# Performance work log

Measured on AMD Instinct MI355X. Metric: run time of the kernel, lower is better.

The kernel has to match this reference:

```python
import jax, jax.numpy as jnp
import numpy as np

NUM_EXPERTS = 4096
NUM_KEYS = 64  # floor(sqrt(num_experts))
TOP_K = 16
NORM_TOPK = False
BN_EPS = 1e-5


def setup_inputs() -> dict:
    key = jax.random.key(0)
    ks = jax.random.split(key, 7)
    B, S, H, I = 2, 2048, 2048, 8192
    s = 0.02
    return {
        "hidden_states": jax.random.normal(ks[0], (B, S, H), jnp.float32),
        "router_gate_w": jax.random.normal(ks[1], (2 * NUM_KEYS, H), jnp.float32) * s,
        "down_embed": jax.random.normal(ks[2], (NUM_EXPERTS, H), jnp.float32) * s,
        "up_embed": jax.random.normal(ks[3], (NUM_EXPERTS, H), jnp.float32) * s,
        "gate_w": jax.random.normal(ks[4], (I, H), jnp.float32) * s,
        "up_w": jax.random.normal(ks[5], (I, H), jnp.float32) * s,
        "down_w": jax.random.normal(ks[6], (H, I), jnp.float32) * s,
    }


def reference(hidden_states, router_gate_w, down_embed, up_embed, gate_w, up_w, down_w):
    B, S, H = hidden_states.shape
    x = hidden_states.reshape(-1, H)  # [N, H]

    # BatchNorm1d(affine=False), training-mode batch statistics (biased var)
    mu = jnp.mean(x, axis=0, keepdims=True)
    var = jnp.mean(jnp.square(x - mu), axis=0, keepdims=True)
    xn = (x - mu) * jax.lax.rsqrt(var + BN_EPS)

    # product-key router: logits [2, N, num_keys]
    rlog = (xn @ router_gate_w.T).reshape(-1, 2, NUM_KEYS).transpose(1, 0, 2)
    logp = jax.nn.log_softmax(rlog, axis=-1)

    # full product scores [N, nk, nk]; top-k over nk*nk candidates
    full = logp[0][:, :, None] + logp[1][:, None, :]
    scores, indices = jax.lax.top_k(full.reshape(-1, NUM_KEYS * NUM_KEYS), TOP_K)
    routing_weights = jnp.exp(scores)  # [N, k]
    if NORM_TOPK:
        routing_weights = routing_weights / jnp.sum(routing_weights, axis=-1, keepdims=True)

    # PEER-style expert: scalar key match then weighted up-embedding sum
    d = down_embed[indices]  # [N, k, H]
    u = up_embed[indices]    # [N, k, H]
    h = jnp.einsum('nh,nkh->nk', x, d)
    experts_states = jnp.einsum('nk,nk,nkh->nh', routing_weights, h, u)

    # dense gated MLP (silu)
    mlp = (jax.nn.silu(x @ gate_w.T) * (x @ up_w.T)) @ down_w.T

    out = (mlp + experts_states).reshape(B, S, H)
    return out, rlog
```

## Files before the change

### kernel.cpp

```cpp
#include <hip/hip_runtime.h>
#include <stdint.h>

#define H_DIM 2048
#define N_TOK 4096
#define I_DIM 8192

typedef __attribute__((ext_vector_type(8))) short short8;
typedef __attribute__((ext_vector_type(4))) float f32x4;

typedef const __attribute__((address_space(1))) unsigned int* gp_t;
typedef __attribute__((address_space(3))) unsigned int* lp_t;

__device__ __forceinline__ void gload16(const unsigned short* g, short* l) {
    __builtin_amdgcn_global_load_lds((gp_t)g, (lp_t)l, 16, 0, 0);
}

__device__ __forceinline__ unsigned short f2bf(float f) {
    union { float f; unsigned int u; } c; c.f = f;
    unsigned int u = c.u;
    return (unsigned short)((u + 0x7FFFu + ((u >> 16) & 1u)) >> 16);
}
__device__ __forceinline__ float bf2f(unsigned short u) {
    union { unsigned int i; float f; } c; c.i = ((unsigned int)u) << 16;
    return c.f;
}

__device__ __forceinline__ float wmax64(float v) {
#pragma unroll
    for (int o = 32; o > 0; o >>= 1) v = fmaxf(v, __shfl_xor(v, o));
    return v;
}
__device__ __forceinline__ float wsum64(float v) {
#pragma unroll
    for (int o = 32; o > 0; o >>= 1) v += __shfl_xor(v, o);
    return v;
}

template<int K, int RSTEP, int LSTEP>
__device__ __forceinline__ void stage4(const unsigned short* src, short* dst) {
#pragma unroll
    for (int j = 0; j < 4; ++j)
        gload16(src + (size_t)j * RSTEP * K, dst + j * LSTEP);
}

__global__ __launch_bounds__(256) void bn_stats(const float* __restrict__ x,
                                                float* __restrict__ ps, float* __restrict__ pq) {
    int col = blockIdx.x * 256 + threadIdx.x;
    int r0  = blockIdx.y * 128;
    float s = 0.f, q = 0.f;
    for (int r = 0; r < 128; ++r) {
        float v = x[(size_t)(r0 + r) * H_DIM + col];
        s += v; q += v * v;
    }
    ps[blockIdx.y * H_DIM + col] = s;
    pq[blockIdx.y * H_DIM + col] = q;
}

__global__ __launch_bounds__(256) void bn_finalize(const float* __restrict__ ps, const float* __restrict__ pq,
                                                   float* __restrict__ mu, float* __restrict__ rsig) {
    int c = blockIdx.x * 256 + threadIdx.x;
    float s = 0.f, q = 0.f;
    for (int i = 0; i < 32; ++i) { s += ps[i * H_DIM + c]; q += pq[i * H_DIM + c]; }
    float m = s * (1.f / N_TOK);
    float v = q * (1.f / N_TOK) - m * m;
    mu[c] = m;
    rsig[c] = rsqrtf(v + 1e-5f);
}

__global__ __launch_bounds__(256) void cvt_x(const float* __restrict__ x, unsigned short* __restrict__ xb) {
    size_t i = ((size_t)blockIdx.x * 256 + threadIdx.x) * 4;
    float4 v = *(const float4*)(x + i);
    uint2 o;
    o.x = (unsigned)f2bf(v.x) | ((unsigned)f2bf(v.y) << 16);
    o.y = (unsigned)f2bf(v.z) | ((unsigned)f2bf(v.w) << 16);
    *(uint2*)(xb + i) = o;
}

__global__ __launch_bounds__(256) void cvt_w(const float* __restrict__ src, unsigned short* __restrict__ dst) {
    size_t off = ((size_t)blockIdx.x * 256 + threadIdx.x) * 8;
    float4 a = *(const float4*)(src + off);
    float4 b = *(const float4*)(src + off + 4);
    short8 s;
    s[0]=(short)f2bf(a.x); s[1]=(short)f2bf(a.y); s[2]=(short)f2bf(a.z); s[3]=(short)f2bf(a.w);
    s[4]=(short)f2bf(b.x); s[5]=(short)f2bf(b.y); s[6]=(short)f2bf(b.z); s[7]=(short)f2bf(b.w);
    *(short8*)(dst + off) = s;
}

__global__ __launch_bounds__(256) void router_kernel(const float* __restrict__ x, const float* __restrict__ rgw,
                                                     const float* __restrict__ mu, const float* __restrict__ rsig,
                                                     float* __restrict__ rlog) {
    __shared__ float xs[16][65];
    __shared__ float rs[128][65];
    const int t = threadIdx.x;
    const int n0 = blockIdx.x * 16;
    const int tk = t >> 5;
    const int jj = t & 31;
    float acc[2][4] = {{0.f,0.f,0.f,0.f},{0.f,0.f,0.f,0.f}};

    for (int kc = 0; kc < H_DIM; kc += 64) {
        {
            int row = t >> 4, c4 = (t & 15) * 4;
            float4 v = *(const float4*)(x + (size_t)(n0 + row) * H_DIM + kc + c4);
            float4 m = *(const float4*)(mu + kc + c4);
            float4 r = *(const float4*)(rsig + kc + c4);
            xs[row][c4 + 0] = (v.x - m.x) * r.x;
            xs[row][c4 + 1] = (v.y - m.y) * r.y;
            xs[row][c4 + 2] = (v.z - m.z) * r.z;
            xs[row][c4 + 3] = (v.w - m.w) * r.w;
        }
        {
            int row = t >> 1, base = (t & 1) * 32;
            const float* src = rgw + (size_t)row * H_DIM + kc + base;
#pragma unroll
            for (int i = 0; i < 8; ++i) {
                float4 v = *(const float4*)(src + i * 4);
                rs[row][base + i*4 + 0] = v.x;
                rs[row][base + i*4 + 1] = v.y;
                rs[row][base + i*4 + 2] = v.z;
                rs[row][base + i*4 + 3] = v.w;
            }
        }
        __syncthreads();
#pragma unroll 4
        for (int k = 0; k < 64; ++k) {
            float x0 = xs[tk][k], x1 = xs[tk + 8][k];
            float r0 = rs[jj][k], r1 = rs[jj + 32][k], r2 = rs[jj + 64][k], r3 = rs[jj + 96][k];
            acc[0][0] += x0 * r0; acc[0][1] += x0 * r1; acc[0][2] += x0 * r2; acc[0][3] += x0 * r3;
            acc[1][0] += x1 * r0; acc[1][1] += x1 * r1; acc[1][2] += x1 * r2; acc[1][3] += x1 * r3;
        }
        __syncthreads();
    }
#pragma unroll
    for (int a = 0; a < 2; ++a)
#pragma unroll
        for (int b = 0; b < 4; ++b) {
            int n = n0 + tk + 8 * a;
            int j = jj + 32 * b;
            rlog[(size_t)(j >> 6) * (N_TOK * 64) + (size_t)n * 64 + (j & 63)] = acc[a][b];
        }
}

__global__ __launch_bounds__(256) void topk_kernel(const float* __restrict__ rlog,
                                                   float* __restrict__ topw, int* __restrict__ topi) {
    const int lane = threadIdx.x & 63;
    const int n = blockIdx.x * 4 + (threadIdx.x >> 6);

    float a = rlog[(size_t)n * 64 + lane];
    float b = rlog[(size_t)(N_TOK * 64) + (size_t)n * 64 + lane];
    float ma = wmax64(a);
    float lpa = a - ma - logf(wsum64(expf(a - ma)));
    float mb = wmax64(b);
    float lpb = b - mb - logf(wsum64(expf(b - mb)));

    float va = lpa, vb = lpb;
    float tva = -1e30f, tvb = -1e30f; int tia = 0, tib = 0;
    for (int it = 0; it < 16; ++it) {
        float mx = wmax64(va);
        int w = __ffsll(__ballot(va == mx)) - 1;
        if (lane == it) { tva = mx; tia = w; }
        if (lane == w) va = -1e30f;
        mx = wmax64(vb);
        w = __ffsll(__ballot(vb == mx)) - 1;
        if (lane == it) { tvb = mx; tib = w; }
        if (lane == w) vb = -1e30f;
    }
    float av = __shfl(tva, lane >> 2);
    int   ai = __shfl(tia, lane >> 2);
    int   q0 = (lane & 3) * 4;
    float c0 = av + __shfl(tvb, q0 + 0); int b0 = __shfl(tib, q0 + 0);
    float c1 = av + __shfl(tvb, q0 + 1); int b1 = __shfl(tib, q0 + 1);
    float c2 = av + __shfl(tvb, q0 + 2); int b2 = __shfl(tib, q0 + 2);
    float c3 = av + __shfl(tvb, q0 + 3); int b3 = __shfl(tib, q0 + 3);

    for (int it = 0; it < 16; ++it) {
        float lv = c0; int lq = 0;
        if (c1 > lv) { lv = c1; lq = 1; }
        if (c2 > lv) { lv = c2; lq = 2; }
        if (c3 > lv) { lv = c3; lq = 3; }
        float mx = wmax64(lv);
        int w = __ffsll(__ballot(lv == mx)) - 1;
        if (lane == w) {
            int bj;
            switch (lq) {
                case 0:  bj = b0; c0 = -1e30f; break;
                case 1:  bj = b1; c1 = -1e30f; break;
                case 2:  bj = b2; c2 = -1e30f; break;
                default: bj = b3; c3 = -1e30f; break;
            }
            topw[n * 16 + it] = expf(mx);
            topi[n * 16 + it] = ai * 64 + bj;
        }
    }
}

__global__ __launch_bounds__(256) void experts_kernel(const float* __restrict__ x, const float* __restrict__ de,
                                                      const float* __restrict__ ue, const float* __restrict__ topw,
                                                      const int* __restrict__ topi, float* __restrict__ out) {
    __shared__ float psum[16][4];
    const int n = blockIdx.x;
    const int t = threadIdx.x, lane = t & 63, wid = t >> 6;

    float xr[8];
    {
        float4 v0 = *(const float4*)(x + (size_t)n * H_DIM + t * 8);
        float4 v1 = *(const float4*)(x + (size_t)n * H_DIM + t * 8 + 4);
        xr[0]=v0.x; xr[1]=v0.y; xr[2]=v0.z; xr[3]=v0.w;
        xr[4]=v1.x; xr[5]=v1.y; xr[6]=v1.z; xr[7]=v1.w;
    }
    int   eidx[16];
    float ew[16];
#pragma unroll
    for (int k = 0; k < 16; ++k) { eidx[k] = topi[n * 16 + k]; ew[k] = topw[n * 16 + k]; }

#pragma unroll
    for (int k = 0; k < 16; ++k) {
        const float* dr = de + (size_t)eidx[k] * H_DIM + t * 8;
        float4 v0 = *(const float4*)dr;
        float4 v1 = *(const float4*)(dr + 4);
        float p = v0.x*xr[0] + v0.y*xr[1] + v0.z*xr[2] + v0.w*xr[3]
                + v1.x*xr[4] + v1.y*xr[5] + v1.z*xr[6] + v1.w*xr[7];
        p = wsum64(p);
        if (lane == 0) psum[k][wid] = p;
    }
    __syncthreads();

    float acc[8] = {0,0,0,0,0,0,0,0};
#pragma unroll
    for (int k = 0; k < 16; ++k) {
        float h = psum[k][0] + psum[k][1] + psum[k][2] + psum[k][3];
        float coef = ew[k] * h;
        const float* ur = ue + (size_t)eidx[k] * H_DIM + t * 8;
        float4 v0 = *(const float4*)ur;
        float4 v1 = *(const float4*)(ur + 4);
        acc[0] += coef * v0.x; acc[1] += coef * v0.y; acc[2] += coef * v0.z; acc[3] += coef * v0.w;
        acc[4] += coef * v1.x; acc[5] += coef * v1.y; acc[6] += coef * v1.z; acc[7] += coef * v1.w;
    }
    float4 o0 = {acc[0], acc[1], acc[2], acc[3]};
    float4 o1 = {acc[4], acc[5], acc[6], acc[7]};
    *(float4*)(out + (size_t)n * H_DIM + t * 8)     = o0;
    *(float4*)(out + (size_t)n * H_DIM + t * 8 + 4) = o1;
}

#define SWZB(row, byteoff) ((byteoff) ^ (((row) & 7) << 4))

#define NT256 (H_DIM / 64)

__global__ __launch_bounds__(512, 2) void gemm256(const unsigned short* __restrict__ Amat,
                                                  const unsigned short* __restrict__ Bmat,
                                                  unsigned short* __restrict__ act, int mode) {
    __shared__ __attribute__((aligned(16))) short sA[2][16384];
    __shared__ __attribute__((aligned(16))) short sB[2][16384];
    const int t = threadIdx.x;
    const int lane = t & 63, wid = t >> 6;
    const int wm = wid >> 2, wn = wid & 3;
    const int l15 = lane & 15, l4 = lane >> 4;
    const int bid = blockIdx.x;
    const int sw = (bid & 7) * 64 + (bid >> 3);
    const int bx = sw & 31, by = sw >> 5;
    const int row0 = by * 256, col0 = bx * 256;

    const int rseg = lane >> 3;
    const int chunk = (lane & 7) ^ rseg;
    const unsigned short* aSrc = Amat + (size_t)(row0 + wid * 8 + rseg) * H_DIM + chunk * 8;
    const unsigned short* bSrc = Bmat + (size_t)(col0 + wid * 8 + rseg) * H_DIM + chunk * 8;

    const int swzb = (l15 & 7) << 4;
    const int kx0 = (l4 * 16) ^ swzb;
    const int kx1 = (64 + l4 * 16) ^ swzb;
    const int arow = (wm * 128 + l15) * 64;
    const int brow = (wn * 64 + l15) * 64;

    f32x4 zero = {0.f, 0.f, 0.f, 0.f};
    f32x4 acc[8][4];
#pragma unroll
    for (int m = 0; m < 8; ++m)
#pragma unroll
        for (int n = 0; n < 4; ++n) acc[m][n] = zero;

    stage4<H_DIM, 64, 4096>(aSrc,      &sA[0][wid * 512]);
    stage4<H_DIM, 64, 4096>(bSrc,      &sB[0][wid * 512]);
    stage4<H_DIM, 64, 4096>(aSrc + 64, &sA[1][wid * 512]);
    stage4<H_DIM, 64, 4096>(bSrc + 64, &sB[1][wid * 512]);
    asm volatile("s_waitcnt vmcnt(8)" ::: "memory");
    __builtin_amdgcn_s_barrier();
    asm volatile("" ::: "memory");

    for (int g = 0; g < NT256; ++g) {
        const int c = g & 1;
        const short* Ac = &sA[c][0];
        const short* Bc = &sB[c][0];
        short8 a0[4], a0h[4], a1[4], a1h[4], b0[4], b1[4];
#pragma unroll
        for (int m = 0; m < 4; ++m) a0[m]  = *(const short8*)(Ac + arow + m * 1024 + (kx0 >> 1));
#pragma unroll
        for (int m = 0; m < 4; ++m) a0h[m] = *(const short8*)(Ac + arow + (m + 4) * 1024 + (kx0 >> 1));
#pragma unroll
        for (int n = 0; n < 4; ++n) b0[n]  = *(const short8*)(Bc + brow + n * 1024 + (kx0 >> 1));
        __builtin_amdgcn_s_setprio(1);
#pragma unroll
        for (int m = 0; m < 4; ++m)
#pragma unroll
            for (int n = 0; n < 4; ++n)
                acc[m][n] = __builtin_amdgcn_mfma_f32_16x16x32_bf16(a0[m], b0[n], acc[m][n], 0, 0, 0);
        __builtin_amdgcn_s_setprio(0);
        asm volatile("" ::: "memory");
        __builtin_amdgcn_s_barrier();
        asm volatile("" ::: "memory");
#pragma unroll
        for (int m = 0; m < 4; ++m) a1[m]  = *(const short8*)(Ac + arow + m * 1024 + (kx1 >> 1));
#pragma unroll
        for (int m = 0; m < 4; ++m) a1h[m] = *(const short8*)(Ac + arow + (m + 4) * 1024 + (kx1 >> 1));
#pragma unroll
        for (int n = 0; n < 4; ++n) b1[n]  = *(const short8*)(Bc + brow + n * 1024 + (kx1 >> 1));
        __builtin_amdgcn_s_setprio(1);
#pragma unroll
        for (int m = 0; m < 4; ++m)
#pragma unroll
            for (int n = 0; n < 4; ++n)
                acc[m + 4][n] = __builtin_amdgcn_mfma_f32_16x16x32_bf16(a0h[m], b0[n], acc[m + 4][n], 0, 0, 0);
        __builtin_amdgcn_s_setprio(0);
        asm volatile("s_waitcnt lgkmcnt(0)" ::: "memory");
        __builtin_amdgcn_s_barrier();
        asm volatile("" ::: "memory");
        if (g + 2 < NT256) stage4<H_DIM, 64, 4096>(aSrc + (size_t)(g + 2) * 64, &sA[c][wid * 512]);
        __builtin_amdgcn_s_setprio(1);
#pragma unroll
        for (int m = 0; m < 4; ++m)
#pragma unroll
            for (int n = 0; n < 4; ++n)
                acc[m][n] = __builtin_amdgcn_mfma_f32_16x16x32_bf16(a1[m], b1[n], acc[m][n], 0, 0, 0);
        __builtin_amdgcn_s_setprio(0);
        asm volatile("" ::: "memory");
        __builtin_amdgcn_s_barrier();
        asm volatile("" ::: "memory");
        if (g + 2 < NT256) stage4<H_DIM, 64, 4096>(bSrc + (size_t)(g + 2) * 64, &sB[c][wid * 512]);
        __builtin_amdgcn_s_setprio(1);
#pragma unroll
        for (int m = 0; m < 4; ++m)
#pragma unroll
            for (int n = 0; n < 4; ++n)
                acc[m + 4][n] = __builtin_amdgcn_mfma_f32_16x16x32_bf16(a1h[m], b1[n], acc[m + 4][n], 0, 0, 0);
        __builtin_amdgcn_s_setprio(0);
        if (g + 2 < NT256) { asm volatile("s_waitcnt vmcnt(8)" ::: "memory"); }
        else               { asm volatile("s_waitcnt vmcnt(0)" ::: "memory"); }
        __builtin_amdgcn_s_barrier();
        asm volatile("" ::: "memory");
    }

    const int rbase = row0 + wm * 128, cbase = col0 + wn * 64;
    if (mode == 0) {
#pragma unroll
        for (int m = 0; m < 8; ++m)
#pragma unroll
            for (int n = 0; n < 4; ++n)
#pragma unroll
                for (int j = 0; j < 4; ++j) {
                    int r = rbase + m * 16 + l4 * 4 + j;
                    int c2 = cbase + n * 16 + l15;
                    act[(size_t)r * I_DIM + c2] = f2bf(acc[m][n][j]);
                }
    } else {
#pragma unroll
        for (int m = 0; m < 8; ++m)
#pragma unroll
            for (int n = 0; n < 4; ++n)
#pragma unroll
                for (int j = 0; j < 4; ++j) {
                    int r = rbase + m * 16 + l4 * 4 + j;
                    int c2 = cbase + n * 16 + l15;
                    size_t idx = (size_t)r * I_DIM + c2;
                    float gv = bf2f(act[idx]);
                    float uv = acc[m][n][j];
                    float sv = gv / (1.f + expf(-gv));
                    act[idx] = f2bf(sv * uv);
                }
    }
}

#define NTD (I_DIM / 64)

__global__ __launch_bounds__(256, 2) void gemm_down128(const unsigned short* __restrict__ act,
                                                       const unsigned short* __restrict__ dwb,
                                                       float* __restrict__ out) {
    __shared__ __attribute__((aligned(16))) short sA[2][8192];
    __shared__ __attribute__((aligned(16))) short sB[2][8192];
    const int t = threadIdx.x;
    const int lane = t & 63, wid = t >> 6;
    const int wm = wid >> 1, wn = wid & 1;
    const int l15 = lane & 15, l4 = lane >> 4;
    const int bid = blockIdx.x;
    const int sw = (bid & 7) * 64 + (bid >> 3);
    const int bx = sw & 15, by = sw >> 4;
    const int row0 = by * 128, col0 = bx * 128;

    const int rseg = lane >> 3;
    const int chunk = (lane & 7) ^ rseg;
    const unsigned short* aSrc = act + (size_t)(row0 + wid * 8 + rseg) * I_DIM + chunk * 8;
    const unsigned short* bSrc = dwb + (size_t)(col0 + wid * 8 + rseg) * I_DIM + chunk * 8;

    const int swzb = (l15 & 7) << 4;
    const int kx0 = (l4 * 16) ^ swzb;
    const int kx1 = (64 + l4 * 16) ^ swzb;
    const int arow = (wm * 64 + l15) * 64;
    const int brow = (wn * 64 + l15) * 64;

    f32x4 zero = {0.f, 0.f, 0.f, 0.f};
    f32x4 acc[4][4];
#pragma unroll
    for (int m = 0; m < 4; ++m)
#pragma unroll
        for (int n = 0; n < 4; ++n) acc[m][n] = zero;

    stage4<I_DIM, 32, 2048>(aSrc,      &sA[0][wid * 512]);
    stage4<I_DIM, 32, 2048>(bSrc,      &sB[0][wid * 512]);
    stage4<I_DIM, 32, 2048>(aSrc + 64, &sA[1][wid * 512]);
    stage4<I_DIM, 32, 2048>(bSrc + 64, &sB[1][wid * 512]);
    asm volatile("s_waitcnt vmcnt(8)" ::: "memory");
    __builtin_amdgcn_s_barrier();
    asm volatile("" ::: "memory");

    for (int g = 0; g < NTD; ++g) {
        const int c = g & 1;
        const short* Ac = &sA[c][0];
        const short* Bc = &sB[c][0];
        short8 a0[4], a1[4], b0[4], b1[4];
#pragma unroll
        for (int m = 0; m < 4; ++m) a0[m] = *(const short8*)(Ac + arow + m * 1024 + (kx0 >> 1));
#pragma unroll
        for (int n = 0; n < 4; ++n) b0[n] = *(const short8*)(Bc + brow + n * 1024 + (kx0 >> 1));
#pragma unroll
        for (int m = 0; m < 4; ++m) a1[m] = *(const short8*)(Ac + arow + m * 1024 + (kx1 >> 1));
#pragma unroll
        for (int n = 0; n < 4; ++n) b1[n] = *(const short8*)(Bc + brow + n * 1024 + (kx1 >> 1));
        __builtin_amdgcn_s_setprio(1);
#pragma unroll
        for (int m = 0; m < 4; ++m)
#pragma unroll
            for (int n = 0; n < 4; ++n)
                acc[m][n] = __builtin_amdgcn_mfma_f32_16x16x32_bf16(a0[m], b0[n], acc[m][n], 0, 0, 0);
        __builtin_amdgcn_s_setprio(0);
        asm volatile("s_waitcnt lgkmcnt(0)" ::: "memory");
        __builtin_amdgcn_s_barrier();
        asm volatile("" ::: "memory");
        if (g + 2 < NTD) {
            stage4<I_DIM, 32, 2048>(aSrc + (size_t)(g + 2) * 64, &sA[c][wid * 512]);
            stage4<I_DIM, 32, 2048>(bSrc + (size_t)(g + 2) * 64, &sB[c][wid * 512]);
        }
        __builtin_amdgcn_s_setprio(1);
#pragma unroll
        for (int m = 0; m < 4; ++m)
#pragma unroll
            for (int n = 0; n < 4; ++n)
                acc[m][n] = __builtin_amdgcn_mfma_f32_16x16x32_bf16(a1[m], b1[n], acc[m][n], 0, 0, 0);
        __builtin_amdgcn_s_setprio(0);
        if (g + 2 < NTD) { asm volatile("s_waitcnt vmcnt(8)" ::: "memory"); }
        else             { asm volatile("s_waitcnt vmcnt(0)" ::: "memory"); }
        __builtin_amdgcn_s_barrier();
        asm volatile("" ::: "memory");
    }

    const int rbase = row0 + wm * 64, cbase = col0 + wn * 64;
#pragma unroll
    for (int m = 0; m < 4; ++m)
#pragma unroll
        for (int n = 0; n < 4; ++n)
#pragma unroll
            for (int j = 0; j < 4; ++j) {
                int r = rbase + m * 16 + l4 * 4 + j;
                int c2 = cbase + n * 16 + l15;
                out[(size_t)r * H_DIM + c2] += acc[m][n][j];
            }
}

__global__ __launch_bounds__(256) void gemm_gu(const unsigned short* __restrict__ xb,
                                               const float* __restrict__ gw, const float* __restrict__ uw,
                                               unsigned short* __restrict__ act) {
    __shared__ __attribute__((aligned(16))) short As[128 * 64];
    __shared__ __attribute__((aligned(16))) short Bg[128 * 64];
    __shared__ __attribute__((aligned(16))) short Bu[128 * 64];
    const int t = threadIdx.x;
    const int lane = t & 63, wid = t >> 6;
    const int wr = wid >> 1, wc = wid & 1;
    const int l15 = lane & 15, l4 = lane >> 4;
    const int row0 = blockIdx.y * 128;
    const int col0 = blockIdx.x * 128;
    const int srow = t >> 1, shalf = (t & 1) * 32;

    f32x4 zero = {0.f, 0.f, 0.f, 0.f};
    f32x4 accg[4][4], accu[4][4];
#pragma unroll
    for (int m = 0; m < 4; ++m)
#pragma unroll
        for (int n = 0; n < 4; ++n) { accg[m][n] = zero; accu[m][n] = zero; }

    for (int kt = 0; kt < H_DIM; kt += 64) {
        {
            const unsigned short* src = xb + (size_t)(row0 + srow) * H_DIM + kt + shalf;
#pragma unroll
            for (int i = 0; i < 4; ++i) {
                int boff = SWZB(srow, (shalf + i * 8) * 2);
                *(short8*)(As + srow * 64 + (boff >> 1)) = *(const short8*)(src + i * 8);
            }
        }
        {
            const float* g = gw + (size_t)(col0 + srow) * H_DIM + kt + shalf;
            const float* u = uw + (size_t)(col0 + srow) * H_DIM + kt + shalf;
#pragma unroll
            for (int i = 0; i < 4; ++i) {
                int boff = SWZB(srow, (shalf + i * 8) * 2);
                float4 a0 = *(const float4*)(g + i * 8);
                float4 a1 = *(const float4*)(g + i * 8 + 4);
                short8 s;
                s[0]=(short)f2bf(a0.x); s[1]=(short)f2bf(a0.y); s[2]=(short)f2bf(a0.z); s[3]=(short)f2bf(a0.w);
                s[4]=(short)f2bf(a1.x); s[5]=(short)f2bf(a1.y); s[6]=(short)f2bf(a1.z); s[7]=(short)f2bf(a1.w);
                *(short8*)(Bg + srow * 64 + (boff >> 1)) = s;
                float4 b0 = *(const float4*)(u + i * 8);
                float4 b1 = *(const float4*)(u + i * 8 + 4);
                short8 r;
                r[0]=(short)f2bf(b0.x); r[1]=(short)f2bf(b0.y); r[2]=(short)f2bf(b0.z); r[3]=(short)f2bf(b0.w);
                r[4]=(short)f2bf(b1.x); r[5]=(short)f2bf(b1.y); r[6]=(short)f2bf(b1.z); r[7]=(short)f2bf(b1.w);
                *(short8*)(Bu + srow * 64 + (boff >> 1)) = r;
            }
        }
        __syncthreads();
#pragma unroll
        for (int kk = 0; kk < 64; kk += 32) {
            short8 af[4], bgf[4], buf_[4];
#pragma unroll
            for (int m = 0; m < 4; ++m) {
                int row = wr * 64 + m * 16 + l15;
                af[m] = *(const short8*)(As + row * 64 + (SWZB(row, (kk + l4 * 8) * 2) >> 1));
            }
#pragma unroll
            for (int n = 0; n < 4; ++n) {
                int row = wc * 64 + n * 16 + l15;
                int off = row * 64 + (SWZB(row, (kk + l4 * 8) * 2) >> 1);
                bgf[n]  = *(const short8*)(Bg + off);
                buf_[n] = *(const short8*)(Bu + off);
            }
#pragma unroll
            for (int m = 0; m < 4; ++m)
#pragma unroll
                for (int n = 0; n < 4; ++n) {
                    accg[m][n] = __builtin_amdgcn_mfma_f32_16x16x32_bf16(af[m], bgf[n],  accg[m][n], 0, 0, 0);
                    accu[m][n] = __builtin_amdgcn_mfma_f32_16x16x32_bf16(af[m], buf_[n], accu[m][n], 0, 0, 0);
                }
        }
        __syncthreads();
    }
    const int rbase = row0 + wr * 64, cbase = col0 + wc * 64;
#pragma unroll
    for (int m = 0; m < 4; ++m)
#pragma unroll
        for (int n = 0; n < 4; ++n)
#pragma unroll
            for (int j = 0; j < 4; ++j) {
                int r = rbase + m * 16 + l4 * 4 + j;
                int c = cbase + n * 16 + l15;
                float gv = accg[m][n][j];
                float uv = accu[m][n][j];
                float sv = gv / (1.f + expf(-gv));
                act[(size_t)r * I_DIM + c] = f2bf(sv * uv);
            }
}

__global__ __launch_bounds__(256) void gemm_down(const unsigned short* __restrict__ act,
                                                 const float* __restrict__ dw, float* __restrict__ out) {
    __shared__ __attribute__((aligned(16))) short As[128 * 64];
    __shared__ __attribute__((aligned(16))) short Bs[128 * 64];
    const int t = threadIdx.x;
    const int lane = t & 63, wid = t >> 6;
    const int wr = wid >> 1, wc = wid & 1;
    const int l15 = lane & 15, l4 = lane >> 4;
    const int row0 = blockIdx.y * 128;
    const int col0 = blockIdx.x * 128;
    const int srow = t >> 1, shalf = (t & 1) * 32;

    f32x4 zero = {0.f, 0.f, 0.f, 0.f};
    f32x4 acc[4][4];
#pragma unroll
    for (int m = 0; m < 4; ++m)
#pragma unroll
        for (int n = 0; n < 4; ++n) acc[m][n] = zero;

    for (int kt = 0; kt < I_DIM; kt += 64) {
        {
            const unsigned short* src = act + (size_t)(row0 + srow) * I_DIM + kt + shalf;
#pragma unroll
            for (int i = 0; i < 4; ++i) {
                int boff = SWZB(srow, (shalf + i * 8) * 2);
                *(short8*)(As + srow * 64 + (boff >> 1)) = *(const short8*)(src + i * 8);
            }
        }
        {
            const float* g = dw + (size_t)(col0 + srow) * I_DIM + kt + shalf;
#pragma unroll
            for (int i = 0; i < 4; ++i) {
                int boff = SWZB(srow, (shalf + i * 8) * 2);
                float4 a0 = *(const float4*)(g + i * 8);
                float4 a1 = *(const float4*)(g + i * 8 + 4);
                short8 s;
                s[0]=(short)f2bf(a0.x); s[1]=(short)f2bf(a0.y); s[2]=(short)f2bf(a0.z); s[3]=(short)f2bf(a0.w);
                s[4]=(short)f2bf(a1.x); s[5]=(short)f2bf(a1.y); s[6]=(short)f2bf(a1.z); s[7]=(short)f2bf(a1.w);
                *(short8*)(Bs + srow * 64 + (boff >> 1)) = s;
            }
        }
        __syncthreads();
#pragma unroll
        for (int kk = 0; kk < 64; kk += 32) {
            short8 af[4], bf[4];
#pragma unroll
            for (int m = 0; m < 4; ++m) {
                int row = wr * 64 + m * 16 + l15;
                af[m] = *(const short8*)(As + row * 64 + (SWZB(row, (kk + l4 * 8) * 2) >> 1));
            }
#pragma unroll
            for (int n = 0; n < 4; ++n) {
                int row = wc * 64 + n * 16 + l15;
                bf[n] = *(const short8*)(Bs + row * 64 + (SWZB(row, (kk + l4 * 8) * 2) >> 1));
            }
#pragma unroll
            for (int m = 0; m < 4; ++m)
#pragma unroll
                for (int n = 0; n < 4; ++n)
                    acc[m][n] = __builtin_amdgcn_mfma_f32_16x16x32_bf16(af[m], bf[n], acc[m][n], 0, 0, 0);
        }
        __syncthreads();
    }
    const int rbase = row0 + wr * 64, cbase = col0 + wc * 64;
#pragma unroll
    for (int m = 0; m < 4; ++m)
#pragma unroll
        for (int n = 0; n < 4; ++n)
#pragma unroll
            for (int j = 0; j < 4; ++j) {
                int r = rbase + m * 16 + l4 * 4 + j;
                int c = cbase + n * 16 + l15;
                out[(size_t)r * H_DIM + c] += acc[m][n][j];
            }
}

extern "C" void kernel_launch(void* const* d_in, const int* in_sizes, int n_in,
                              void* d_out, int out_size, void* d_ws, size_t ws_size,
                              hipStream_t stream) {
    const float* x   = (const float*)d_in[0];
    const float* rgw = (const float*)d_in[1];
    const float* de  = (const float*)d_in[2];
    const float* ue  = (const float*)d_in[3];
    const float* gw  = (const float*)d_in[4];
    const float* uw  = (const float*)d_in[5];
    const float* dw  = (const float*)d_in[6];
    float* out = (float*)d_out;
    char* ws = (char*)d_ws;

    float* ps   = (float*)(ws + 0);
    float* pq   = (float*)(ws + 262144);
    float* mu   = (float*)(ws + 524288);
    float* rsig = (float*)(ws + 532480);
    float* topw = (float*)(ws + 540672);
    int*   topi = (int*)  (ws + 802816);
    unsigned short* xb  = (unsigned short*)(ws + 1179648);
    unsigned short* act = (unsigned short*)(ws + 17956864);
    unsigned short* gwb = (unsigned short*)(ws + 85065728);
    unsigned short* uwb = (unsigned short*)(ws + 118620160);
    unsigned short* dwb = (unsigned short*)(ws + 152174592);
    float* rlog = out + 8388608;
    const bool fast = ws_size >= 185729024ULL;

    bn_stats   <<<dim3(8, 32), 256, 0, stream>>>(x, ps, pq);
    bn_finalize<<<8, 256, 0, stream>>>(ps, pq, mu, rsig);
    cvt_x      <<<8192, 256, 0, stream>>>(x, xb);
    router_kernel<<<256, 256, 0, stream>>>(x, rgw, mu, rsig, rlog);
    topk_kernel<<<1024, 256, 0, stream>>>(rlog, topw, topi);
    experts_kernel<<<4096, 256, 0, stream>>>(x, de, ue, topw, topi, out);

    if (fast) {
        cvt_w<<<8192, 256, 0, stream>>>(gw, gwb);
        cvt_w<<<8192, 256, 0, stream>>>(uw, uwb);
        cvt_w<<<8192, 256, 0, stream>>>(dw, dwb);
        gemm256<<<512, 512, 0, stream>>>(xb, gwb, act, 0);
        gemm256<<<512, 512, 0, stream>>>(xb, uwb, act, 1);
        gemm_down128<<<512, 256, 0, stream>>>(act, dwb, out);
    } else {
        gemm_gu    <<<dim3(64, 32), 256, 0, stream>>>(xb, gw, uw, act);
        gemm_down  <<<dim3(16, 32), 256, 0, stream>>>(act, dw, out);
    }
}
```

Measured before the change: 846.1 us.

## Fuse bf16 conversions, use bf16 expert embeddings, simplify GEMM double buffering

Merges all fp32-to-bf16 conversions (weights, expert embeddings, x) into one launch. Adds a bf16 variant of the experts kernel that gathers down/up embeddings at half the bytes. Replaces the hand-scheduled two-stage-ahead prefetch with split barriers in the gate/up and down GEMMs with a simpler one-ahead double buffer and __syncthreads. The simpler pipeline may hide less load latency, and the extra embedding conversion adds traffic and lowers expert precision.

```diff
diff --git a/kernel.cpp b/kernel.cpp
--- a/kernel.cpp
+++ b/kernel.cpp
@@ -65,6 +65,29 @@
     float v = q * (1.f / N_TOK) - m * m;
     mu[c] = m;
     rsig[c] = rsqrtf(v + 1e-5f);
+}
+
+__global__ __launch_bounds__(256) void cvt_all(const float* __restrict__ gw, const float* __restrict__ uw,
+                                               const float* __restrict__ dw, const float* __restrict__ de,
+                                               const float* __restrict__ ue, const float* __restrict__ x,
+                                               unsigned short* __restrict__ gwb, unsigned short* __restrict__ uwb,
+                                               unsigned short* __restrict__ dwb, unsigned short* __restrict__ deb,
+                                               unsigned short* __restrict__ ueb, unsigned short* __restrict__ xb) {
+    int b = blockIdx.x;
+    const float* src; unsigned short* dst; size_t base;
+    if      (b < 8192)  { src = gw; dst = gwb; base = (size_t)b; }
+    else if (b < 16384) { src = uw; dst = uwb; base = (size_t)(b - 8192); }
+    else if (b < 24576) { src = dw; dst = dwb; base = (size_t)(b - 16384); }
+    else if (b < 28672) { src = de; dst = deb; base = (size_t)(b - 24576); }
+    else if (b < 32768) { src = ue; dst = ueb; base = (size_t)(b - 28672); }
+    else                { src = x;  dst = xb;  base = (size_t)(b - 32768); }
+    size_t off = (base * 256 + threadIdx.x) * 8;
+    float4 a = *(const float4*)(src + off);
+    float4 c = *(const float4*)(src + off + 4);
+    short8 s;
+    s[0]=(short)f2bf(a.x); s[1]=(short)f2bf(a.y); s[2]=(short)f2bf(a.z); s[3]=(short)f2bf(a.w);
+    s[4]=(short)f2bf(c.x); s[5]=(short)f2bf(c.y); s[6]=(short)f2bf(c.z); s[7]=(short)f2bf(c.w);
+    *(short8*)(dst + off) = s;
 }
 
 __global__ __launch_bounds__(256) void cvt_x(const float* __restrict__ x, unsigned short* __restrict__ xb) {
@@ -193,6 +216,51 @@
     }
 }
 
+__global__ __launch_bounds__(256) void experts_kernel_b(const float* __restrict__ x, const unsigned short* __restrict__ de,
+                                                        const unsigned short* __restrict__ ue, const float* __restrict__ topw,
+                                                        const int* __restrict__ topi, float* __restrict__ out) {
+    __shared__ float psum[16][4];
+    const int n = blockIdx.x;
+    const int t = threadIdx.x, lane = t & 63, wid = t >> 6;
+
+    float xr[8];
+    {
+        float4 v0 = *(const float4*)(x + (size_t)n * H_DIM + t * 8);
+        float4 v1 = *(const float4*)(x + (size_t)n * H_DIM + t * 8 + 4);
+        xr[0]=v0.x; xr[1]=v0.y; xr[2]=v0.z; xr[3]=v0.w;
+        xr[4]=v1.x; xr[5]=v1.y; xr[6]=v1.z; xr[7]=v1.w;
+    }
+    int   eidx[16];
+    float ew[16];
+#pragma unroll
+    for (int k = 0; k < 16; ++k) { eidx[k] = topi[n * 16 + k]; ew[k] = topw[n * 16 + k]; }
+
+#pragma unroll
+    for (int k = 0; k < 16; ++k) {
+        short8 d = *(const short8*)(de + (size_t)eidx[k] * H_DIM + t * 8);
+        float p = 0.f;
+#pragma unroll
+        for (int j = 0; j < 8; ++j) p += bf2f((unsigned short)d[j]) * xr[j];
+        p = wsum64(p);
+        if (lane == 0) psum[k][wid] = p;
+    }
+    __syncthreads();
+
+    float acc[8] = {0,0,0,0,0,0,0,0};
+#pragma unroll
+    for (int k = 0; k < 16; ++k) {
+        float h = psum[k][0] + psum[k][1] + psum[k][2] + psum[k][3];
+        float coef = ew[k] * h;
+        short8 u = *(const short8*)(ue + (size_t)eidx[k] * H_DIM + t * 8);
+#pragma unroll
+        for (int j = 0; j < 8; ++j) acc[j] += coef * bf2f((unsigned short)u[j]);
+    }
+    float4 o0 = {acc[0], acc[1], acc[2], acc[3]};
+    float4 o1 = {acc[4], acc[5], acc[6], acc[7]};
+    *(float4*)(out + (size_t)n * H_DIM + t * 8)     = o0;
+    *(float4*)(out + (size_t)n * H_DIM + t * 8 + 4) = o1;
+}
+
 __global__ __launch_bounds__(256) void experts_kernel(const float* __restrict__ x, const float* __restrict__ de,
                                                       const float* __restrict__ ue, const float* __restrict__ topw,
                                                       const int* __restrict__ topi, float* __restrict__ out) {
@@ -277,74 +345,62 @@
 #pragma unroll
         for (int n = 0; n < 4; ++n) acc[m][n] = zero;
 
-    stage4<H_DIM, 64, 4096>(aSrc,      &sA[0][wid * 512]);
-    stage4<H_DIM, 64, 4096>(bSrc,      &sB[0][wid * 512]);
-    stage4<H_DIM, 64, 4096>(aSrc + 64, &sA[1][wid * 512]);
-    stage4<H_DIM, 64, 4096>(bSrc + 64, &sB[1][wid * 512]);
-    asm volatile("s_waitcnt vmcnt(8)" ::: "memory");
-    __builtin_amdgcn_s_barrier();
-    asm volatile("" ::: "memory");
-
+    stage4<H_DIM, 64, 4096>(aSrc, &sA[0][wid * 512]);
+    stage4<H_DIM, 64, 4096>(bSrc, &sB[0][wid * 512]);
+    __syncthreads();
+
+    int cur = 0;
     for (int g = 0; g < NT256; ++g) {
-        const int c = g & 1;
-        const short* Ac = &sA[c][0];
-        const short* Bc = &sB[c][0];
-        short8 a0[4], a0h[4], a1[4], a1h[4], b0[4], b1[4];
-#pragma unroll
-        for (int m = 0; m < 4; ++m) a0[m]  = *(const short8*)(Ac + arow + m * 1024 + (kx0 >> 1));
-#pragma unroll
-        for (int m = 0; m < 4; ++m) a0h[m] = *(const short8*)(Ac + arow + (m + 4) * 1024 + (kx0 >> 1));
-#pragma unroll
-        for (int n = 0; n < 4; ++n) b0[n]  = *(const short8*)(Bc + brow + n * 1024 + (kx0 >> 1));
-        __builtin_amdgcn_s_setprio(1);
-#pragma unroll
-        for (int m = 0; m < 4; ++m)
-#pragma unroll
-            for (int n = 0; n < 4; ++n)
-                acc[m][n] = __builtin_amdgcn_mfma_f32_16x16x32_bf16(a0[m], b0[n], acc[m][n], 0, 0, 0);
-        __builtin_amdgcn_s_setprio(0);
-        asm volatile("" ::: "memory");
-        __builtin_amdgcn_s_barrier();
-        asm volatile("" ::: "memory");
-#pragma unroll
-        for (int m = 0; m < 4; ++m) a1[m]  = *(const short8*)(Ac + arow + m * 1024 + (kx1 >> 1));
-#pragma unroll
-        for (int m = 0; m < 4; ++m) a1h[m] = *(const short8*)(Ac + arow + (m + 4) * 1024 + (kx1 >> 1));
-#pragma unroll
-        for (int n = 0; n < 4; ++n) b1[n]  = *(const short8*)(Bc + brow + n * 1024 + (kx1 >> 1));
-        __builtin_amdgcn_s_setprio(1);
-#pragma unroll
-        for (int m = 0; m < 4; ++m)
-#pragma unroll
-            for (int n = 0; n < 4; ++n)
-                acc[m + 4][n] = __builtin_amdgcn_mfma_f32_16x16x32_bf16(a0h[m], b0[n], acc[m + 4][n], 0, 0, 0);
-        __builtin_amdgcn_s_setprio(0);
-        asm volatile("s_waitcnt lgkmcnt(0)" ::: "memory");
-        __builtin_amdgcn_s_barrier();
-        asm volatile("" ::: "memory");
-        if (g + 2 < NT256) stage4<H_DIM, 64, 4096>(aSrc + (size_t)(g + 2) * 64, &sA[c][wid * 512]);
-        __builtin_amdgcn_s_setprio(1);
-#pragma unroll
-        for (int m = 0; m < 4; ++m)
-#pragma unroll
-            for (int n = 0; n < 4; ++n)
-                acc[m][n] = __builtin_amdgcn_mfma_f32_16x16x32_bf16(a1[m], b1[n], acc[m][n], 0, 0, 0);
-        __builtin_amdgcn_s_setprio(0);
-        asm volatile("" ::: "memory");
-        __builtin_amdgcn_s_barrier();
-        asm volatile("" ::: "memory");
-        if (g + 2 < NT256) stage4<H_DIM, 64, 4096>(bSrc + (size_t)(g + 2) * 64, &sB[c][wid * 512]);
-        __builtin_amdgcn_s_setprio(1);
-#pragma unroll
-        for (int m = 0; m < 4; ++m)
-#pragma unroll
-            for (int n = 0; n < 4; ++n)
-                acc[m + 4][n] = __builtin_amdgcn_mfma_f32_16x16x32_bf16(a1h[m], b1[n], acc[m + 4][n], 0, 0, 0);
-        __builtin_amdgcn_s_setprio(0);
-        if (g + 2 < NT256) { asm volatile("s_waitcnt vmcnt(8)" ::: "memory"); }
-        else               { asm volatile("s_waitcnt vmcnt(0)" ::: "memory"); }
-        __builtin_amdgcn_s_barrier();
-        asm volatile("" ::: "memory");
+        if (g + 1 < NT256) {
+            stage4<H_DIM, 64, 4096>(aSrc + (size_t)(g + 1) * 64, &sA[cur ^ 1][wid * 512]);
+            stage4<H_DIM, 64, 4096>(bSrc + (size_t)(g + 1) * 64, &sB[cur ^ 1][wid * 512]);
+        }
+        const short* Ac = &sA[cur][0];
+        const short* Bc = &sB[cur][0];
+        {
+            short8 a0[4], a0h[4], b0[4];
+#pragma unroll
+            for (int m = 0; m < 4; ++m) a0[m]  = *(const short8*)(Ac + arow + m * 1024 + (kx0 >> 1));
+#pragma unroll
+            for (int m = 0; m < 4; ++m) a0h[m] = *(const short8*)(Ac + arow + (m + 4) * 1024 + (kx0 >> 1));
+#pragma unroll
+            for (int n = 0; n < 4; ++n) b0[n]  = *(const short8*)(Bc + brow + n * 1024 + (kx0 >> 1));
+            __builtin_amdgcn_s_setprio(1);
+#pragma unroll
+            for (int m = 0; m < 4; ++m)
+#pragma unroll
+                for (int n = 0; n < 4; ++n)
+                    acc[m][n] = __builtin_amdgcn_mfma_f32_16x16x32_bf16(a0[m], b0[n], acc[m][n], 0, 0, 0);
+#pragma unroll
+            for (int m = 0; m < 4; ++m)
+#pragma unroll
+                for (int n = 0; n < 4; ++n)
+                    acc[m + 4][n] = __builtin_amdgcn_mfma_f32_16x16x32_bf16(a0h[m], b0[n], acc[m + 4][n], 0, 0, 0);
+            __builtin_amdgcn_s_setprio(0);
+        }
+        {
+            short8 a1[4], a1h[4], b1[4];
+#pragma unroll
+            for (int m = 0; m < 4; ++m) a1[m]  = *(const short8*)(Ac + arow + m * 1024 + (kx1 >> 1));
+#pragma unroll
+            for (int m = 0; m < 4; ++m) a1h[m] = *(const short8*)(Ac + arow + (m + 4) * 1024 + (kx1 >> 1));
+#pragma unroll
+            for (int n = 0; n < 4; ++n) b1[n]  = *(const short8*)(Bc + brow + n * 1024 + (kx1 >> 1));
+            __builtin_amdgcn_s_setprio(1);
+#pragma unroll
+            for (int m = 0; m < 4; ++m)
+#pragma unroll
+                for (int n = 0; n < 4; ++n)
+                    acc[m][n] = __builtin_amdgcn_mfma_f32_16x16x32_bf16(a1[m], b1[n], acc[m][n], 0, 0, 0);
+#pragma unroll
+            for (int m = 0; m < 4; ++m)
+#pragma unroll
+                for (int n = 0; n < 4; ++n)
+                    acc[m + 4][n] = __builtin_amdgcn_mfma_f32_16x16x32_bf16(a1h[m], b1[n], acc[m + 4][n], 0, 0, 0);
+            __builtin_amdgcn_s_setprio(0);
+        }
+        __syncthreads();
+        cur ^= 1;
     }
 
     const int rbase = row0 + wm * 128, cbase = col0 + wn * 64;
@@ -411,52 +467,48 @@
 #pragma unroll
         for (int n = 0; n < 4; ++n) acc[m][n] = zero;
 
-    stage4<I_DIM, 32, 2048>(aSrc,      &sA[0][wid * 512]);
-    stage4<I_DIM, 32, 2048>(bSrc,      &sB[0][wid * 512]);
-    stage4<I_DIM, 32, 2048>(aSrc + 64, &sA[1][wid * 512]);
-    stage4<I_DIM, 32, 2048>(bSrc + 64, &sB[1][wid * 512]);
-    asm volatile("s_waitcnt vmcnt(8)" ::: "memory");
-    __builtin_amdgcn_s_barrier();
-    asm volatile("" ::: "memory");
-
+    stage4<I_DIM, 32, 2048>(aSrc, &sA[0][wid * 512]);
+    stage4<I_DIM, 32, 2048>(bSrc, &sB[0][wid * 512]);
+    __syncthreads();
+
+    int cur = 0;
     for (int g = 0; g < NTD; ++g) {
-        const int c = g & 1;
-        const short* Ac = &sA[c][0];
-        const short* Bc = &sB[c][0];
-        short8 a0[4], a1[4], b0[4], b1[4];
-#pragma unroll
-        for (int m = 0; m < 4; ++m) a0[m] = *(const short8*)(Ac + arow + m * 1024 + (kx0 >> 1));
-#pragma unroll
-        for (int n = 0; n < 4; ++n) b0[n] = *(const short8*)(Bc + brow + n * 1024 + (kx0 >> 1));
-#pragma unroll
-        for (int m = 0; m < 4; ++m) a1[m] = *(const short8*)(Ac + arow + m * 1024 + (kx1 >> 1));
-#pragma unroll
-        for (int n = 0; n < 4; ++n) b1[n] = *(const short8*)(Bc + brow + n * 1024 + (kx1 >> 1));
-        __builtin_amdgcn_s_setprio(1);
-#pragma unroll
-        for (int m = 0; m < 4; ++m)
-#pragma unroll
-            for (int n = 0; n < 4; ++n)
-                acc[m][n] = __builtin_amdgcn_mfma_f32_16x16x32_bf16(a0[m], b0[n], acc[m][n], 0, 0, 0);
-        __builtin_amdgcn_s_setprio(0);
-        asm volatile("s_waitcnt lgkmcnt(0)" ::: "memory");
-        __builtin_amdgcn_s_barrier();
-        asm volatile("" ::: "memory");
-        if (g + 2 < NTD) {
-            stage4<I_DIM, 32, 2048>(aSrc + (size_t)(g + 2) * 64, &sA[c][wid * 512]);
-            stage4<I_DIM, 32, 2048>(bSrc + (size_t)(g + 2) * 64, &sB[c][wid * 512]);
-        }
-        __builtin_amdgcn_s_setprio(1);
-#pragma unroll
-        for (int m = 0; m < 4; ++m)
-#pragma unroll
-            for (int n = 0; n < 4; ++n)
-                acc[m][n] = __builtin_amdgcn_mfma_f32_16x16x32_bf16(a1[m], b1[n], acc[m][n], 0, 0, 0);
-        __builtin_amdgcn_s_setprio(0);
-        if (g + 2 < NTD) { asm volatile("s_waitcnt vmcnt(8)" ::: "memory"); }
-        else             { asm volatile("s_waitcnt vmcnt(0)" ::: "memory"); }
-        __builtin_amdgcn_s_barrier();
-        asm volatile("" ::: "memory");
+        if (g + 1 < NTD) {
+            stage4<I_DIM, 32, 2048>(aSrc + (size_t)(g + 1) * 64, &sA[cur ^ 1][wid * 512]);
+            stage4<I_DIM, 32, 2048>(bSrc + (size_t)(g + 1) * 64, &sB[cur ^ 1][wid * 512]);
+        }
+        const short* Ac = &sA[cur][0];
+        const short* Bc = &sB[cur][0];
+        {
+            short8 a0[4], b0[4];
+#pragma unroll
+            for (int m = 0; m < 4; ++m) a0[m] = *(const short8*)(Ac + arow + m * 1024 + (kx0 >> 1));
+#pragma unroll
+            for (int n = 0; n < 4; ++n) b0[n] = *(const short8*)(Bc + brow + n * 1024 + (kx0 >> 1));
+            __builtin_amdgcn_s_setprio(1);
+#pragma unroll
+            for (int m = 0; m < 4; ++m)
+#pragma unroll
+                for (int n = 0; n < 4; ++n)
+                    acc[m][n] = __builtin_amdgcn_mfma_f32_16x16x32_bf16(a0[m], b0[n], acc[m][n], 0, 0, 0);
+            __builtin_amdgcn_s_setprio(0);
+        }
+        {
+            short8 a1[4], b1[4];
+#pragma unroll
+            for (int m = 0; m < 4; ++m) a1[m] = *(const short8*)(Ac + arow + m * 1024 + (kx1 >> 1));
+#pragma unroll
+            for (int n = 0; n < 4; ++n) b1[n] = *(const short8*)(Bc + brow + n * 1024 + (kx1 >> 1));
+            __builtin_amdgcn_s_setprio(1);
+#pragma unroll
+            for (int m = 0; m < 4; ++m)
+#pragma unroll
+                for (int n = 0; n < 4; ++n)
+                    acc[m][n] = __builtin_amdgcn_mfma_f32_16x16x32_bf16(a1[m], b1[n], acc[m][n], 0, 0, 0);
+            __builtin_amdgcn_s_setprio(0);
+        }
+        __syncthreads();
+        cur ^= 1;
     }
 
     const int rbase = row0 + wm * 64, cbase = col0 + wn * 64;
@@ -664,25 +716,36 @@
     unsigned short* gwb = (unsigned short*)(ws + 85065728);
     unsigned short* uwb = (unsigned short*)(ws + 118620160);
     unsigned short* dwb = (unsigned short*)(ws + 152174592);
+    unsigned short* deb = (unsigned short*)(ws + 185729024);
+    unsigned short* ueb = (unsigned short*)(ws + 202506240);
     float* rlog = out + 8388608;
-    const bool fast = ws_size >= 185729024ULL;
+    const bool fast  = ws_size >= 185729024ULL;
+    const bool fast2 = ws_size >= 219283456ULL;
 
     bn_stats   <<<dim3(8, 32), 256, 0, stream>>>(x, ps, pq);
     bn_finalize<<<8, 256, 0, stream>>>(ps, pq, mu, rsig);
-    cvt_x      <<<8192, 256, 0, stream>>>(x, xb);
     router_kernel<<<256, 256, 0, stream>>>(x, rgw, mu, rsig, rlog);
     topk_kernel<<<1024, 256, 0, stream>>>(rlog, topw, topi);
-    experts_kernel<<<4096, 256, 0, stream>>>(x, de, ue, topw, topi, out);
-
-    if (fast) {
+
+    if (fast2) {
+        cvt_all<<<36864, 256, 0, stream>>>(gw, uw, dw, de, ue, x, gwb, uwb, dwb, deb, ueb, xb);
+        experts_kernel_b<<<4096, 256, 0, stream>>>(x, deb, ueb, topw, topi, out);
+        gemm256<<<512, 512, 0, stream>>>(xb, gwb, act, 0);
+        gemm256<<<512, 512, 0, stream>>>(xb, uwb, act, 1);
+        gemm_down128<<<512, 256, 0, stream>>>(act, dwb, out);
+    } else if (fast) {
+        cvt_x<<<8192, 256, 0, stream>>>(x, xb);
         cvt_w<<<8192, 256, 0, stream>>>(gw, gwb);
         cvt_w<<<8192, 256, 0, stream>>>(uw, uwb);
         cvt_w<<<8192, 256, 0, stream>>>(dw, dwb);
+        experts_kernel<<<4096, 256, 0, stream>>>(x, de, ue, topw, topi, out);
         gemm256<<<512, 512, 0, stream>>>(xb, gwb, act, 0);
         gemm256<<<512, 512, 0, stream>>>(xb, uwb, act, 1);
         gemm_down128<<<512, 256, 0, stream>>>(act, dwb, out);
     } else {
-        gemm_gu    <<<dim3(64, 32), 256, 0, stream>>>(xb, gw, uw, act);
-        gemm_down  <<<dim3(16, 32), 256, 0, stream>>>(act, dw, out);
-    }
-}
+        cvt_x<<<8192, 256, 0, stream>>>(x, xb);
+        experts_kernel<<<4096, 256, 0, stream>>>(x, de, ue, topw, topi, out);
+        gemm_gu  <<<dim3(64, 32), 256, 0, stream>>>(xb, gw, uw, act);
+        gemm_down<<<dim3(16, 32), 256, 0, stream>>>(act, dw, out);
+    }
+}
```

Result: faster. 768.9 us (-9.1%).
